# Optimization experiments

Hardware: AMD Instinct MI355X
Metric: run time of the kernel (lower is better)

The kernel has to match this reference:

```python
import jax, jax.numpy as jnp
import numpy as np
from jax.ops import segment_sum

N_NODES = 100000
N_EDGES = 1600000

def setup_inputs() -> dict:
    key = jax.random.key(0)
    ks = jax.random.split(key, 16)
    s = 0.1
    return {
        "x": jax.random.normal(ks[0], (N_NODES, 8), jnp.float32),
        "edge_index": jax.random.randint(ks[1], (2, N_EDGES), 0, N_NODES, jnp.int32),
        "W1l": jax.random.normal(ks[2], (8, 128)) * s,
        "W1r": jax.random.normal(ks[3], (8, 128)) * s,
        "b1": jnp.zeros((128,)),
        "W2l": jax.random.normal(ks[4], (128, 128)) * s,
        "W2r": jax.random.normal(ks[5], (128, 128)) * s,
        "b2": jnp.zeros((128,)),
        "W3l": jax.random.normal(ks[6], (128, 1)) * s,
        "W3r": jax.random.normal(ks[7], (128, 1)) * s,
        "b3": jnp.zeros((1,)),
        "Ta1_W": jax.random.normal(ks[8], (4, 8, 8)) * s,
        "Ta1_b": jnp.zeros((8,)),
        "Ta2_W": jax.random.normal(ks[9], (4, 8, 1)) * s,
        "Ta2_b": jnp.zeros((1,)),
        "Tb1_W": jax.random.normal(ks[10], (10, 8, 8)) * s,
        "Tb1_b": jnp.zeros((8,)),
        "Tb2_W": jax.random.normal(ks[11], (10, 8, 1)) * s,
        "Tb2_b": jnp.zeros((1,)),
        "lin2_W": jax.random.normal(ks[12], (2, 1)) * s,
        "lin2_b": jnp.zeros((1,)),
        "lin1_W": jax.random.normal(ks[13], (2, 1)) * s,
        "lin1_b": jnp.zeros((1,)),
    }

def reference(x, edge_index, W1l, W1r, b1, W2l, W2r, b2, W3l, W3r, b3,
              Ta1_W, Ta1_b, Ta2_W, Ta2_b, Tb1_W, Tb1_b, Tb2_W, Tb2_b,
              lin2_W, lin2_b, lin1_W, lin1_b):
    N = x.shape[0]
    src, dst = edge_index[0], edge_index[1]  # message flows src -> dst

    # in-degree of each target node (edge weight = 1)
    deg = segment_sum(jnp.ones_like(src, dtype=x.dtype), dst, num_segments=N)

    # --- SAGEConv: lin_l(mean_{j in N(i)} x_j) + lin_r(x_i) + bias ---
    inv_deg = jnp.where(deg > 0, 1.0 / jnp.maximum(deg, 1.0), 0.0)
    def sage(h, Wl, Wr, b):
        agg = segment_sum(h[src], dst, num_segments=N) * inv_deg[:, None]
        return agg @ Wl + h @ Wr + b

    # --- TAGConv: sym-normalized adjacency powers, no self loops ---
    dinv = jnp.where(deg > 0, jax.lax.rsqrt(jnp.maximum(deg, 1.0)), 0.0)
    norm = dinv[src] * dinv[dst]  # [E]
    def tag(h, Ws, b):  # Ws: [K+1, in, out]
        out = h @ Ws[0]
        for k in range(1, Ws.shape[0]):
            h = segment_sum(h[src] * norm[:, None], dst, num_segments=N)
            out = out + h @ Ws[k]
        return out + b

    relu = jax.nn.relu
    x1 = relu(sage(x, W1l, W1r, b1))
    x1 = relu(sage(x1, W2l, W2r, b2))
    x1 = relu(sage(x1, W3l, W3r, b3))

    x2 = relu(tag(x, Ta1_W, Ta1_b))
    x2 = relu(tag(x2, Ta2_W, Ta2_b))

    x3 = relu(tag(x, Tb1_W, Tb1_b))
    x3 = relu(tag(x3, Tb2_W, Tb2_b))

    x23 = relu(jnp.concatenate([x2, x3], axis=1) @ lin2_W + lin2_b)
    out = relu(jnp.concatenate([x1, x23], axis=1) @ lin1_W + lin1_b)
    return out
```

## Files before the change

### kernel.cpp

```cpp
#include <hip/hip_runtime.h>

#define NN 100000
#define NE 1600000
#define TPB 256

__global__ void k_init(int* __restrict__ deg, int* __restrict__ cursor, int* __restrict__ counter) {
    int i = blockIdx.x * TPB + threadIdx.x;
    if (i < NN) { deg[i] = 0; cursor[i] = 0; }
    if (i == 0) counter[0] = 0;
}

__global__ void k_deg(const int* __restrict__ dst, int* __restrict__ deg) {
    int e = blockIdx.x * TPB + threadIdx.x;
    if (e < NE) atomicAdd(&deg[dst[e]], 1);
}

__global__ void k_prep(const int* __restrict__ deg, float* __restrict__ inv_deg,
                       float* __restrict__ dinv, int* __restrict__ row_start,
                       int* __restrict__ counter) {
    int i = blockIdx.x * TPB + threadIdx.x;
    if (i < NN) {
        int d = deg[i];
        inv_deg[i] = d > 0 ? 1.0f / (float)d : 0.0f;
        dinv[i]    = d > 0 ? 1.0f / sqrtf((float)d) : 0.0f;
        row_start[i] = atomicAdd(counter, d);
    }
}

__global__ void k_fill(const int* __restrict__ src, const int* __restrict__ dst,
                       const int* __restrict__ row_start, int* __restrict__ cursor,
                       int* __restrict__ col) {
    int e = blockIdx.x * TPB + threadIdx.x;
    if (e < NE) {
        int d = dst[e];
        int p = atomicAdd(&cursor[d], 1);
        col[row_start[d] + p] = src[e];
    }
}

__global__ void k_meanprop8(const float* __restrict__ h, const int* __restrict__ row_start,
                            const int* __restrict__ deg, const float* __restrict__ inv_deg,
                            const int* __restrict__ col, float* __restrict__ out) {
    int t = blockIdx.x * TPB + threadIdx.x;
    if (t >= NN * 2) return;
    int n = t >> 1, half = t & 1;
    int rs = row_start[n], end = rs + deg[n];
    const float4* h4 = (const float4*)h;
    float4 s0 = make_float4(0,0,0,0), s1 = make_float4(0,0,0,0);
    int e = rs + half;
    for (; e + 2 < end; e += 4) {
        int c0 = col[e] * 2, c1 = col[e + 2] * 2;
        float4 a0 = h4[c0], a1 = h4[c0 + 1], b0 = h4[c1], b1 = h4[c1 + 1];
        s0.x += a0.x + b0.x; s0.y += a0.y + b0.y; s0.z += a0.z + b0.z; s0.w += a0.w + b0.w;
        s1.x += a1.x + b1.x; s1.y += a1.y + b1.y; s1.z += a1.z + b1.z; s1.w += a1.w + b1.w;
    }
    if (e < end) {
        int c0 = col[e] * 2;
        float4 a0 = h4[c0], a1 = h4[c0 + 1];
        s0.x += a0.x; s0.y += a0.y; s0.z += a0.z; s0.w += a0.w;
        s1.x += a1.x; s1.y += a1.y; s1.z += a1.z; s1.w += a1.w;
    }
    s0.x += __shfl_xor(s0.x, 1, 64); s0.y += __shfl_xor(s0.y, 1, 64);
    s0.z += __shfl_xor(s0.z, 1, 64); s0.w += __shfl_xor(s0.w, 1, 64);
    s1.x += __shfl_xor(s1.x, 1, 64); s1.y += __shfl_xor(s1.y, 1, 64);
    s1.z += __shfl_xor(s1.z, 1, 64); s1.w += __shfl_xor(s1.w, 1, 64);
    float w = inv_deg[n];
    float4 o = (half == 0) ? s0 : s1;
    o.x *= w; o.y *= w; o.z *= w; o.w *= w;
    ((float4*)out)[n * 2 + half] = o;
}

__global__ void k_meanprop128(const float* __restrict__ h, const int* __restrict__ row_start,
                              const int* __restrict__ deg, const float* __restrict__ inv_deg,
                              const int* __restrict__ col, float* __restrict__ out) {
    int t = blockIdx.x * TPB + threadIdx.x;
    if (t >= NN * 32) return;
    int n = t >> 5, f4 = t & 31;
    int rs = row_start[n], end = rs + deg[n];
    const float4* h4 = (const float4*)h;
    float4 s = make_float4(0.f, 0.f, 0.f, 0.f);
    int e = rs;
    for (; e + 1 < end; e += 2) {
        float4 v0 = h4[(size_t)col[e] * 32 + f4];
        float4 v1 = h4[(size_t)col[e + 1] * 32 + f4];
        s.x += v0.x + v1.x; s.y += v0.y + v1.y;
        s.z += v0.z + v1.z; s.w += v0.w + v1.w;
    }
    if (e < end) {
        float4 v = h4[(size_t)col[e] * 32 + f4];
        s.x += v.x; s.y += v.y; s.z += v.z; s.w += v.w;
    }
    float w = inv_deg[n];
    s.x *= w; s.y *= w; s.z *= w; s.w *= w;
    ((float4*)out)[t] = s;
}

__global__ void k_tagstep(const float* __restrict__ q, const int* __restrict__ row_start,
                          const int* __restrict__ deg, const float* __restrict__ dinv,
                          const int* __restrict__ col, float* __restrict__ qout,
                          const float* __restrict__ Wa, const float* __restrict__ Wb,
                          float* __restrict__ outa, float* __restrict__ outb,
                          const float* __restrict__ ba, const float* __restrict__ bb,
                          int fina, int finb) {
    int t = blockIdx.x * TPB + threadIdx.x;
    if (t >= NN * 4) return;
    int n = t >> 2, qd = t & 3;
    int rs = row_start[n], end = rs + deg[n];
    const float4* q4 = (const float4*)q;
    float4 s0 = make_float4(0,0,0,0), s1 = make_float4(0,0,0,0);
    int e = rs + qd;
    for (; e + 4 < end; e += 8) {
        int c0 = col[e] * 2, c1 = col[e + 4] * 2;
        float4 a0 = q4[c0], a1 = q4[c0 + 1], b0 = q4[c1], b1 = q4[c1 + 1];
        s0.x += a0.x + b0.x; s0.y += a0.y + b0.y; s0.z += a0.z + b0.z; s0.w += a0.w + b0.w;
        s1.x += a1.x + b1.x; s1.y += a1.y + b1.y; s1.z += a1.z + b1.z; s1.w += a1.w + b1.w;
    }
    if (e < end) {
        int c0 = col[e] * 2;
        float4 a0 = q4[c0], a1 = q4[c0 + 1];
        s0.x += a0.x; s0.y += a0.y; s0.z += a0.z; s0.w += a0.w;
        s1.x += a1.x; s1.y += a1.y; s1.z += a1.z; s1.w += a1.w;
    }
    #pragma unroll
    for (int o = 1; o < 4; o <<= 1) {
        s0.x += __shfl_xor(s0.x, o, 64); s0.y += __shfl_xor(s0.y, o, 64);
        s0.z += __shfl_xor(s0.z, o, 64); s0.w += __shfl_xor(s0.w, o, 64);
        s1.x += __shfl_xor(s1.x, o, 64); s1.y += __shfl_xor(s1.y, o, 64);
        s1.z += __shfl_xor(s1.z, o, 64); s1.w += __shfl_xor(s1.w, o, 64);
    }
    float dn = dinv[n];
    float h[8] = { s0.x * dn, s0.y * dn, s0.z * dn, s0.w * dn,
                   s1.x * dn, s1.y * dn, s1.z * dn, s1.w * dn };
    int f0 = qd * 2;
    if (qout) {
        ((float2*)qout)[n * 4 + qd] = make_float2(h[f0] * dn, h[f0 + 1] * dn);
    }
    if (Wa) {
        float2 o = ((float2*)outa)[n * 4 + qd];
        float v0 = o.x, v1 = o.y;
        #pragma unroll
        for (int j = 0; j < 8; ++j) {
            v0 += h[j] * Wa[j * 8 + f0];
            v1 += h[j] * Wa[j * 8 + f0 + 1];
        }
        if (fina) {
            v0 = fmaxf(v0 + ba[f0], 0.f);
            v1 = fmaxf(v1 + ba[f0 + 1], 0.f);
        }
        ((float2*)outa)[n * 4 + qd] = make_float2(v0, v1);
    }
    {
        float2 o = ((float2*)outb)[n * 4 + qd];
        float v0 = o.x, v1 = o.y;
        #pragma unroll
        for (int j = 0; j < 8; ++j) {
            v0 += h[j] * Wb[j * 8 + f0];
            v1 += h[j] * Wb[j * 8 + f0 + 1];
        }
        if (finb) {
            v0 = fmaxf(v0 + bb[f0], 0.f);
            v1 = fmaxf(v1 + bb[f0 + 1], 0.f);
        }
        ((float2*)outb)[n * 4 + qd] = make_float2(v0, v1);
    }
}

__global__ void k_symprop1n(const float* __restrict__ qin, const float* __restrict__ yk,
                            const int* __restrict__ row_start, const int* __restrict__ deg,
                            const float* __restrict__ dinv, const int* __restrict__ col,
                            float* __restrict__ qout, int qstride) {
    int t = blockIdx.x * TPB + threadIdx.x;
    if (t >= NN * 4) return;
    int n = t >> 2, qd = t & 3;
    int rs = row_start[n], d = deg[n];
    float s = 0.f;
    for (int e = rs + qd; e < rs + d; e += 4) s += qin[col[e]];
    s += __shfl_xor(s, 1, 64);
    s += __shfl_xor(s, 2, 64);
    if (qd == 0) {
        float dn = dinv[n];
        qout[(size_t)n * qstride] = dn * (dn * s + yk[n]);
    }
}

__global__ void k_symprop2(const float* __restrict__ q2in, const float* __restrict__ yka,
                           const float* __restrict__ ykb, const int* __restrict__ row_start,
                           const int* __restrict__ deg, const float* __restrict__ dinv,
                           const int* __restrict__ col, float* __restrict__ q2out) {
    int t = blockIdx.x * TPB + threadIdx.x;
    if (t >= NN * 4) return;
    int n = t >> 2, qd = t & 3;
    int rs = row_start[n], d = deg[n];
    const float2* q2 = (const float2*)q2in;
    float sa = 0.f, sb = 0.f;
    for (int e = rs + qd; e < rs + d; e += 4) {
        float2 v = q2[col[e]];
        sa += v.x; sb += v.y;
    }
    sa += __shfl_xor(sa, 1, 64); sa += __shfl_xor(sa, 2, 64);
    sb += __shfl_xor(sb, 1, 64); sb += __shfl_xor(sb, 2, 64);
    if (qd == 0) {
        float dn = dinv[n];
        ((float2*)q2out)[n] = make_float2(dn * (dn * sa + yka[n]),
                                          dn * (dn * sb + ykb[n]));
    }
}

__global__ void k_symprop2fin(const float* __restrict__ q2in, const float* __restrict__ yka,
                              const float* __restrict__ ykb, const int* __restrict__ row_start,
                              const int* __restrict__ deg, const float* __restrict__ dinv,
                              const int* __restrict__ col,
                              const float* __restrict__ biasa, const float* __restrict__ biasb,
                              const float* __restrict__ x1f,
                              const float* __restrict__ l2w, const float* __restrict__ l2b,
                              const float* __restrict__ l1w, const float* __restrict__ l1b,
                              float* __restrict__ out) {
    int t = blockIdx.x * TPB + threadIdx.x;
    if (t >= NN * 4) return;
    int n = t >> 2, qd = t & 3;
    int rs = row_start[n], d = deg[n];
    const float2* q2 = (const float2*)q2in;
    float sa = 0.f, sb = 0.f;
    for (int e = rs + qd; e < rs + d; e += 4) {
        float2 v = q2[col[e]];
        sa += v.x; sb += v.y;
    }
    sa += __shfl_xor(sa, 1, 64); sa += __shfl_xor(sa, 2, 64);
    sb += __shfl_xor(sb, 1, 64); sb += __shfl_xor(sb, 2, 64);
    if (qd == 0) {
        float dn = dinv[n];
        float x2 = fmaxf(dn * sa + yka[n] + biasa[0], 0.f);
        float x3 = fmaxf(dn * sb + ykb[n] + biasb[0], 0.f);
        float x23 = fmaxf(x2 * l2w[0] + x3 * l2w[1] + l2b[0], 0.f);
        out[n] = fmaxf(x1f[n] * l1w[0] + x23 * l1w[1] + l1b[0], 0.f);
    }
}

__global__ void k_red4(const float* __restrict__ ylp, const float* __restrict__ yrp,
                       float* __restrict__ yl, float* __restrict__ yr) {
    int n = blockIdx.x * TPB + threadIdx.x;
    if (n >= NN) return;
    yl[n] = (ylp[n] + ylp[NN + n]) + (ylp[2 * NN + n] + ylp[3 * NN + n]);
    yr[n] = (yrp[n] + yrp[NN + n]) + (yrp[2 * NN + n] + yrp[3 * NN + n]);
}

__global__ void k_sage3(const float* __restrict__ yl, const float* __restrict__ yr,
                        const int* __restrict__ row_start, const int* __restrict__ deg,
                        const float* __restrict__ inv_deg, const int* __restrict__ col,
                        const float* __restrict__ b3, float* __restrict__ x1f) {
    int t = blockIdx.x * TPB + threadIdx.x;
    if (t >= NN * 4) return;
    int n = t >> 2, q = t & 3;
    int rs = row_start[n], d = deg[n];
    float s = 0.f;
    for (int e = rs + q; e < rs + d; e += 4) s += yl[col[e]];
    s += __shfl_xor(s, 1, 64);
    s += __shfl_xor(s, 2, 64);
    if (q == 0) x1f[n] = fmaxf(s * inv_deg[n] + yr[n] + b3[0], 0.f);
}

__global__ void k_sage1(const float* __restrict__ a8, const float* __restrict__ x,
                        const float* __restrict__ W1l, const float* __restrict__ W1r,
                        const float* __restrict__ b1, float* __restrict__ x1) {
    int t = blockIdx.x * TPB + threadIdx.x;
    if (t >= NN * 16) return;
    int n = t >> 4, og = (t & 15) * 8;
    float acc[8];
    #pragma unroll
    for (int j = 0; j < 8; ++j) acc[j] = b1[og + j];
    const float* ar = a8 + (size_t)n * 8;
    const float* xr = x + (size_t)n * 8;
    #pragma unroll
    for (int k = 0; k < 8; ++k) {
        float av = ar[k], xv = xr[k];
        const float4* wl = (const float4*)(W1l + k * 128 + og);
        const float4* wr = (const float4*)(W1r + k * 128 + og);
        float4 l0 = wl[0], l1 = wl[1], r0 = wr[0], r1 = wr[1];
        acc[0] += av * l0.x + xv * r0.x;
        acc[1] += av * l0.y + xv * r0.y;
        acc[2] += av * l0.z + xv * r0.z;
        acc[3] += av * l0.w + xv * r0.w;
        acc[4] += av * l1.x + xv * r1.x;
        acc[5] += av * l1.y + xv * r1.y;
        acc[6] += av * l1.z + xv * r1.z;
        acc[7] += av * l1.w + xv * r1.w;
    }
    #pragma unroll
    for (int j = 0; j < 8; ++j)
        x1[(size_t)n * 128 + og + j] = fmaxf(acc[j], 0.f);
}

__global__ __launch_bounds__(256) void k_transpose(const float* __restrict__ in0,
        float* __restrict__ out0, const float* __restrict__ in1, float* __restrict__ out1) {
    const float* in = blockIdx.y ? in1 : in0;
    float* outp = blockIdx.y ? out1 : out0;
    __shared__ float t[128][65];
    int n0 = blockIdx.x * 64;
    int tid = threadIdx.x;
    #pragma unroll
    for (int i = 0; i < 8; ++i) {
        int idx = tid + i * 256;
        int nl = idx >> 5;
        int kq = (idx & 31) << 2;
        int n = n0 + nl;
        float4 v = (n < NN) ? *(const float4*)(in + (size_t)n * 128 + kq)
                            : make_float4(0.f, 0.f, 0.f, 0.f);
        t[kq][nl] = v.x; t[kq + 1][nl] = v.y; t[kq + 2][nl] = v.z; t[kq + 3][nl] = v.w;
    }
    __syncthreads();
    #pragma unroll
    for (int i = 0; i < 8; ++i) {
        int idx = tid + i * 256;
        int k = idx >> 4;
        int nq = (idx & 15) << 2;
        if (n0 + nq + 3 < NN) {
            float4 v = make_float4(t[k][nq], t[k][nq + 1], t[k][nq + 2], t[k][nq + 3]);
            *(float4*)(outp + (size_t)k * NN + n0 + nq) = v;
        }
    }
}

__global__ __launch_bounds__(256) void k_sage2f(const float* __restrict__ aT,
        const float* __restrict__ xT, const float* __restrict__ W2l,
        const float* __restrict__ W2r, const float* __restrict__ b2,
        const float* __restrict__ W3l, const float* __restrict__ W3r,
        float* __restrict__ ylp, float* __restrict__ yrp) {
    int xcd = blockIdx.x & 7;
    int s = blockIdx.x >> 3;
    int xblk = xcd * 49 + (s >> 2);
    int ogq = s & 3;
    int og = ogq * 32;
    int n0 = xblk * 256 + threadIdx.x;
    int n = (n0 < NN) ? n0 : (NN - 1);
    float acc[32];
    #pragma unroll
    for (int j = 0; j < 32; ++j) acc[j] = b2[og + j];
    const float* ap = aT + n;
    const float* xp = xT + n;
    const float* wlp = W2l + og;
    const float* wrp = W2r + og;
    #pragma unroll 4
    for (int k = 0; k < 128; ++k) {
        float a = ap[0], xv = xp[0];
        ap += NN; xp += NN;
        const float4* wl4 = (const float4*)(wlp + (k << 7));
        const float4* wr4 = (const float4*)(wrp + (k << 7));
        #pragma unroll
        for (int q = 0; q < 8; ++q) {
            float4 wl = wl4[q], wr = wr4[q];
            acc[q * 4 + 0] += a * wl.x + xv * wr.x;
            acc[q * 4 + 1] += a * wl.y + xv * wr.y;
            acc[q * 4 + 2] += a * wl.z + xv * wr.z;
            acc[q * 4 + 3] += a * wl.w + xv * wr.w;
        }
    }
    float pl = 0.f, pr = 0.f;
    #pragma unroll
    for (int j = 0; j < 32; ++j) {
        float v = fmaxf(acc[j], 0.f);
        pl += v * W3l[og + j];
        pr += v * W3r[og + j];
    }
    if (n0 < NN) {
        ylp[(size_t)ogq * NN + n0] = pl;
        yrp[(size_t)ogq * NN + n0] = pr;
    }
}

__global__ void k_taginit(const float* __restrict__ x, const float* __restrict__ TaW,
                          const float* __restrict__ TbW, const float* __restrict__ dinv,
                          float* __restrict__ outa, float* __restrict__ outb,
                          float* __restrict__ q0) {
    int t = blockIdx.x * TPB + threadIdx.x;
    if (t >= NN * 8) return;
    int n = t >> 3, o = t & 7;
    const float* xr = x + (size_t)n * 8;
    float sa = 0.f, sb = 0.f;
    #pragma unroll
    for (int j = 0; j < 8; ++j) {
        float v = xr[j];
        sa += v * TaW[j * 8 + o];
        sb += v * TbW[j * 8 + o];
    }
    outa[t] = sa;
    outb[t] = sb;
    q0[t] = xr[o] * dinv[n];
}

__global__ void k_tag2projAB(const float* __restrict__ outa, const float* __restrict__ outb,
                             const float* __restrict__ TaW2, const float* __restrict__ TbW2,
                             float* __restrict__ ya, float* __restrict__ yb,
                             const float* __restrict__ dinv,
                             float* __restrict__ q2a, float* __restrict__ qb0) {
    int n = blockIdx.x * TPB + threadIdx.x;
    if (n >= NN) return;
    float dn = dinv[n];
    float ha[8], hb[8];
    #pragma unroll
    for (int j = 0; j < 8; ++j) ha[j] = outa[(size_t)n * 8 + j];
    #pragma unroll
    for (int j = 0; j < 8; ++j) hb[j] = outb[(size_t)n * 8 + j];
    #pragma unroll
    for (int k = 0; k < 4; ++k) {
        float s = 0.f;
        #pragma unroll
        for (int j = 0; j < 8; ++j) s += ha[j] * TaW2[k * 8 + j];
        if (k == 3) q2a[(size_t)n * 2] = s * dn;
        else        ya[(size_t)k * NN + n] = s;
    }
    #pragma unroll
    for (int k = 0; k < 10; ++k) {
        float s = 0.f;
        #pragma unroll
        for (int j = 0; j < 8; ++j) s += hb[j] * TbW2[k * 8 + j];
        if (k == 9) qb0[n] = s * dn;
        else        yb[(size_t)k * NN + n] = s;
    }
}

#define GL(kern, n, ...) \
    kern<<<dim3((unsigned)(((long)(n) + TPB - 1) / TPB)), dim3(TPB), 0, stream>>>(__VA_ARGS__)

extern "C" void kernel_launch(void* const* d_in, const int* in_sizes, int n_in,
                              void* d_out, int out_size, void* d_ws, size_t ws_size,
                              hipStream_t stream) {
    (void)in_sizes; (void)n_in; (void)out_size; (void)ws_size;
    const float* x   = (const float*)d_in[0];
    const int*   ei  = (const int*)d_in[1];
    const int*   src = ei;
    const int*   dst = ei + NE;
    const float* W1l = (const float*)d_in[2];
    const float* W1r = (const float*)d_in[3];
    const float* b1  = (const float*)d_in[4];
    const float* W2l = (const float*)d_in[5];
    const float* W2r = (const float*)d_in[6];
    const float* b2  = (const float*)d_in[7];
    const float* W3l = (const float*)d_in[8];
    const float* W3r = (const float*)d_in[9];
    const float* b3  = (const float*)d_in[10];
    const float* TaW1 = (const float*)d_in[11];
    const float* TaB1 = (const float*)d_in[12];
    const float* TaW2 = (const float*)d_in[13];
    const float* TaB2 = (const float*)d_in[14];
    const float* TbW1 = (const float*)d_in[15];
    const float* TbB1 = (const float*)d_in[16];
    const float* TbW2 = (const float*)d_in[17];
    const float* TbB2 = (const float*)d_in[18];
    const float* l2w = (const float*)d_in[19];
    const float* l2b = (const float*)d_in[20];
    const float* l1w = (const float*)d_in[21];
    const float* l1b = (const float*)d_in[22];
    float* out = (float*)d_out;

    char* p = (char*)d_ws;
    size_t off = 0;
    auto alloc = [&](size_t bytes) -> void* {
        void* r = p + off;
        off = (off + bytes + 255) & ~(size_t)255;
        return r;
    };
    int*   deg       = (int*)  alloc((size_t)NN * 4);
    float* inv_deg   = (float*)alloc((size_t)NN * 4);
    float* dinv      = (float*)alloc((size_t)NN * 4);
    int*   row_start = (int*)  alloc((size_t)NN * 4);
    int*   cursor    = (int*)  alloc((size_t)NN * 4);
    int*   counter   = (int*)  alloc(256);
    int*   col       = (int*)  alloc((size_t)NE * 4);
    float* a8        = (float*)alloc((size_t)NN * 8 * 4);
    float* qA        = (float*)alloc((size_t)NN * 8 * 4);
    float* qB        = (float*)alloc((size_t)NN * 8 * 4);
    float* outa      = (float*)alloc((size_t)NN * 8 * 4);
    float* outb      = (float*)alloc((size_t)NN * 8 * 4);
    float* x1        = (float*)alloc((size_t)NN * 128 * 4);
    float* a128      = (float*)alloc((size_t)NN * 128 * 4);
    float* a128T     = (float*)alloc((size_t)NN * 128 * 4);
    float* x1T       = (float*)alloc((size_t)NN * 128 * 4);
    float* ylp       = (float*)alloc((size_t)NN * 4 * 4);
    float* yrp       = (float*)alloc((size_t)NN * 4 * 4);
    float* yl        = (float*)alloc((size_t)NN * 4);
    float* yr        = (float*)alloc((size_t)NN * 4);
    float* x1f       = (float*)alloc((size_t)NN * 4);
    float* tA        = (float*)alloc((size_t)NN * 4);
    float* tB        = (float*)alloc((size_t)NN * 4);
    float* qb0       = (float*)alloc((size_t)NN * 4);
    float* q2a       = (float*)alloc((size_t)NN * 8);
    float* q2b       = (float*)alloc((size_t)NN * 8);
    float* ya        = (float*)alloc((size_t)NN * 4 * 4);
    float* yb        = (float*)alloc((size_t)NN * 10 * 4);

    GL(k_init, NN, deg, cursor, counter);
    GL(k_deg, NE, dst, deg);
    GL(k_prep, NN, deg, inv_deg, dinv, row_start, counter);
    GL(k_fill, NE, src, dst, row_start, cursor, col);

    GL(k_meanprop8, (long)NN * 2, x, row_start, deg, inv_deg, col, a8);
    GL(k_sage1, (long)NN * 16, a8, x, W1l, W1r, b1, x1);
    GL(k_meanprop128, (long)NN * 32, x1, row_start, deg, inv_deg, col, a128);
    k_transpose<<<dim3((NN + 63) / 64, 2), dim3(256), 0, stream>>>(a128, a128T, x1, x1T);
    k_sage2f<<<dim3(1568), dim3(256), 0, stream>>>(a128T, x1T, W2l, W2r, b2, W3l, W3r, ylp, yrp);
    GL(k_red4, NN, ylp, yrp, yl, yr);
    GL(k_sage3, (long)NN * 4, yl, yr, row_start, deg, inv_deg, col, b3, x1f);

    GL(k_taginit, (long)NN * 8, x, TaW1, TbW1, dinv, outa, outb, qA);
    {
        float* qcur = qA;
        float* qnext = qB;
        for (int k = 1; k <= 9; ++k) {
            float* qout = (k < 9) ? qnext : nullptr;
            const float* Wa = (k <= 3) ? (TaW1 + (size_t)k * 64) : nullptr;
            GL(k_tagstep, (long)NN * 4, qcur, row_start, deg, dinv, col, qout,
               Wa, TbW1 + (size_t)k * 64, outa, outb, TaB1, TbB1,
               (k == 3) ? 1 : 0, (k == 9) ? 1 : 0);
            if (qout) { float* tmp = qcur; qcur = qnext; qnext = tmp; }
        }
    }

    GL(k_tag2projAB, NN, outa, outb, TaW2, TbW2, ya, yb, dinv, q2a, qb0);

    GL(k_symprop1n, (long)NN * 4, qb0, yb + 8 * NN, row_start, deg, dinv, col, tA, 1);
    GL(k_symprop1n, (long)NN * 4, tA,  yb + 7 * NN, row_start, deg, dinv, col, tB, 1);
    GL(k_symprop1n, (long)NN * 4, tB,  yb + 6 * NN, row_start, deg, dinv, col, tA, 1);
    GL(k_symprop1n, (long)NN * 4, tA,  yb + 5 * NN, row_start, deg, dinv, col, tB, 1);
    GL(k_symprop1n, (long)NN * 4, tB,  yb + 4 * NN, row_start, deg, dinv, col, tA, 1);
    GL(k_symprop1n, (long)NN * 4, tA,  yb + 3 * NN, row_start, deg, dinv, col, q2a + 1, 2);

    GL(k_symprop2, (long)NN * 4, q2a, ya + 2 * NN, yb + 2 * NN, row_start, deg, dinv, col, q2b);
    GL(k_symprop2, (long)NN * 4, q2b, ya + 1 * NN, yb + 1 * NN, row_start, deg, dinv, col, q2a);
    GL(k_symprop2fin, (long)NN * 4, q2a, ya + 0 * NN, yb + 0 * NN, row_start, deg, dinv, col,
       TaB2, TbB2, x1f, l2w, l2b, l1w, l1b, out);
}
```

Measured before the change: 779.8 us.

## Widen per-node thread groups to 8 lanes and split dense SAGE output groups

The edge-gather kernels (tagstep, symprop, sage3) now assign 8 threads per node instead of 4, which gives more parallelism and memory-level concurrency on the irregular gathers. In tagstep each lane now loads one float4 half rather than both halves. The SAGE2 fused matmul is split into 8 output groups of 16 instead of 4 of 32, doubling the block count and reducing register pressure, at the cost of a larger partial reduction. Row-start assignment in prep now uses a wavefront scan with one atomic per wave instead of one atomic per node.

```diff
diff --git a/kernel.cpp b/kernel.cpp
--- a/kernel.cpp
+++ b/kernel.cpp
@@ -19,11 +19,22 @@
                        float* __restrict__ dinv, int* __restrict__ row_start,
                        int* __restrict__ counter) {
     int i = blockIdx.x * TPB + threadIdx.x;
+    int lane = threadIdx.x & 63;
+    int d = (i < NN) ? deg[i] : 0;
+    int incl = d;
+    #pragma unroll
+    for (int o = 1; o < 64; o <<= 1) {
+        int v = __shfl_up(incl, o, 64);
+        if (lane >= o) incl += v;
+    }
+    int total = __shfl(incl, 63, 64);
+    int base = 0;
+    if (lane == 63) base = atomicAdd(counter, total);
+    base = __shfl(base, 63, 64);
     if (i < NN) {
-        int d = deg[i];
+        row_start[i] = base + incl - d;
         inv_deg[i] = d > 0 ? 1.0f / (float)d : 0.0f;
         dinv[i]    = d > 0 ? 1.0f / sqrtf((float)d) : 0.0f;
-        row_start[i] = atomicAdd(counter, d);
     }
 }
 
@@ -103,65 +114,56 @@
                           const float* __restrict__ ba, const float* __restrict__ bb,
                           int fina, int finb) {
     int t = blockIdx.x * TPB + threadIdx.x;
-    if (t >= NN * 4) return;
-    int n = t >> 2, qd = t & 3;
+    if (t >= NN * 8) return;
+    int n = t >> 3, qd = t & 7;
+    int half = qd & 1, epar = qd >> 1;
     int rs = row_start[n], end = rs + deg[n];
     const float4* q4 = (const float4*)q;
-    float4 s0 = make_float4(0,0,0,0), s1 = make_float4(0,0,0,0);
-    int e = rs + qd;
+    float4 s = make_float4(0,0,0,0);
+    int e = rs + epar;
     for (; e + 4 < end; e += 8) {
-        int c0 = col[e] * 2, c1 = col[e + 4] * 2;
-        float4 a0 = q4[c0], a1 = q4[c0 + 1], b0 = q4[c1], b1 = q4[c1 + 1];
-        s0.x += a0.x + b0.x; s0.y += a0.y + b0.y; s0.z += a0.z + b0.z; s0.w += a0.w + b0.w;
-        s1.x += a1.x + b1.x; s1.y += a1.y + b1.y; s1.z += a1.z + b1.z; s1.w += a1.w + b1.w;
+        int c0 = col[e] * 2 + half, c1 = col[e + 4] * 2 + half;
+        float4 a = q4[c0], b = q4[c1];
+        s.x += a.x + b.x; s.y += a.y + b.y; s.z += a.z + b.z; s.w += a.w + b.w;
     }
     if (e < end) {
-        int c0 = col[e] * 2;
-        float4 a0 = q4[c0], a1 = q4[c0 + 1];
-        s0.x += a0.x; s0.y += a0.y; s0.z += a0.z; s0.w += a0.w;
-        s1.x += a1.x; s1.y += a1.y; s1.z += a1.z; s1.w += a1.w;
-    }
-    #pragma unroll
-    for (int o = 1; o < 4; o <<= 1) {
-        s0.x += __shfl_xor(s0.x, o, 64); s0.y += __shfl_xor(s0.y, o, 64);
-        s0.z += __shfl_xor(s0.z, o, 64); s0.w += __shfl_xor(s0.w, o, 64);
-        s1.x += __shfl_xor(s1.x, o, 64); s1.y += __shfl_xor(s1.y, o, 64);
-        s1.z += __shfl_xor(s1.z, o, 64); s1.w += __shfl_xor(s1.w, o, 64);
+        float4 a = q4[col[e] * 2 + half];
+        s.x += a.x; s.y += a.y; s.z += a.z; s.w += a.w;
+    }
+    #pragma unroll
+    for (int o = 2; o < 8; o <<= 1) {
+        s.x += __shfl_xor(s.x, o, 64); s.y += __shfl_xor(s.y, o, 64);
+        s.z += __shfl_xor(s.z, o, 64); s.w += __shfl_xor(s.w, o, 64);
     }
     float dn = dinv[n];
-    float h[8] = { s0.x * dn, s0.y * dn, s0.z * dn, s0.w * dn,
-                   s1.x * dn, s1.y * dn, s1.z * dn, s1.w * dn };
-    int f0 = qd * 2;
-    if (qout) {
-        ((float2*)qout)[n * 4 + qd] = make_float2(h[f0] * dn, h[f0 + 1] * dn);
-    }
+    float m0 = s.x * dn, m1 = s.y * dn, m2 = s.z * dn, m3 = s.w * dn;
+    if (qout && epar == 0) {
+        ((float4*)qout)[n * 2 + half] = make_float4(m0 * dn, m1 * dn, m2 * dn, m3 * dn);
+    }
+    float o0 = __shfl_xor(m0, 1, 64), o1 = __shfl_xor(m1, 1, 64);
+    float o2 = __shfl_xor(m2, 1, 64), o3 = __shfl_xor(m3, 1, 64);
+    float h[8];
+    if (half) {
+        h[0] = o0; h[1] = o1; h[2] = o2; h[3] = o3;
+        h[4] = m0; h[5] = m1; h[6] = m2; h[7] = m3;
+    } else {
+        h[0] = m0; h[1] = m1; h[2] = m2; h[3] = m3;
+        h[4] = o0; h[5] = o1; h[6] = o2; h[7] = o3;
+    }
+    int f = qd;
     if (Wa) {
-        float2 o = ((float2*)outa)[n * 4 + qd];
-        float v0 = o.x, v1 = o.y;
+        float v = outa[(size_t)n * 8 + f];
         #pragma unroll
-        for (int j = 0; j < 8; ++j) {
-            v0 += h[j] * Wa[j * 8 + f0];
-            v1 += h[j] * Wa[j * 8 + f0 + 1];
-        }
-        if (fina) {
-            v0 = fmaxf(v0 + ba[f0], 0.f);
-            v1 = fmaxf(v1 + ba[f0 + 1], 0.f);
-        }
-        ((float2*)outa)[n * 4 + qd] = make_float2(v0, v1);
+        for (int j = 0; j < 8; ++j) v += h[j] * Wa[j * 8 + f];
+        if (fina) v = fmaxf(v + ba[f], 0.f);
+        outa[(size_t)n * 8 + f] = v;
     }
     {
-        float2 o = ((float2*)outb)[n * 4 + qd];
-        float v0 = o.x, v1 = o.y;
+        float v = outb[(size_t)n * 8 + f];
         #pragma unroll
-        for (int j = 0; j < 8; ++j) {
-            v0 += h[j] * Wb[j * 8 + f0];
-            v1 += h[j] * Wb[j * 8 + f0 + 1];
-        }
-        if (finb) {
-            v0 = fmaxf(v0 + bb[f0], 0.f);
-            v1 = fmaxf(v1 + bb[f0 + 1], 0.f);
-        }
-        ((float2*)outb)[n * 4 + qd] = make_float2(v0, v1);
+        for (int j = 0; j < 8; ++j) v += h[j] * Wb[j * 8 + f];
+        if (finb) v = fmaxf(v + bb[f], 0.f);
+        outb[(size_t)n * 8 + f] = v;
     }
 }
 
@@ -170,13 +172,14 @@
                             const float* __restrict__ dinv, const int* __restrict__ col,
                             float* __restrict__ qout, int qstride) {
     int t = blockIdx.x * TPB + threadIdx.x;
-    if (t >= NN * 4) return;
-    int n = t >> 2, qd = t & 3;
+    if (t >= NN * 8) return;
+    int n = t >> 3, qd = t & 7;
     int rs = row_start[n], d = deg[n];
     float s = 0.f;
-    for (int e = rs + qd; e < rs + d; e += 4) s += qin[col[e]];
+    for (int e = rs + qd; e < rs + d; e += 8) s += qin[col[e]];
     s += __shfl_xor(s, 1, 64);
     s += __shfl_xor(s, 2, 64);
+    s += __shfl_xor(s, 4, 64);
     if (qd == 0) {
         float dn = dinv[n];
         qout[(size_t)n * qstride] = dn * (dn * s + yk[n]);
@@ -188,17 +191,17 @@
                            const int* __restrict__ deg, const float* __restrict__ dinv,
                            const int* __restrict__ col, float* __restrict__ q2out) {
     int t = blockIdx.x * TPB + threadIdx.x;
-    if (t >= NN * 4) return;
-    int n = t >> 2, qd = t & 3;
+    if (t >= NN * 8) return;
+    int n = t >> 3, qd = t & 7;
     int rs = row_start[n], d = deg[n];
     const float2* q2 = (const float2*)q2in;
     float sa = 0.f, sb = 0.f;
-    for (int e = rs + qd; e < rs + d; e += 4) {
+    for (int e = rs + qd; e < rs + d; e += 8) {
         float2 v = q2[col[e]];
         sa += v.x; sb += v.y;
     }
-    sa += __shfl_xor(sa, 1, 64); sa += __shfl_xor(sa, 2, 64);
-    sb += __shfl_xor(sb, 1, 64); sb += __shfl_xor(sb, 2, 64);
+    sa += __shfl_xor(sa, 1, 64); sa += __shfl_xor(sa, 2, 64); sa += __shfl_xor(sa, 4, 64);
+    sb += __shfl_xor(sb, 1, 64); sb += __shfl_xor(sb, 2, 64); sb += __shfl_xor(sb, 4, 64);
     if (qd == 0) {
         float dn = dinv[n];
         ((float2*)q2out)[n] = make_float2(dn * (dn * sa + yka[n]),
@@ -216,17 +219,17 @@
                               const float* __restrict__ l1w, const float* __restrict__ l1b,
                               float* __restrict__ out) {
     int t = blockIdx.x * TPB + threadIdx.x;
-    if (t >= NN * 4) return;
-    int n = t >> 2, qd = t & 3;
+    if (t >= NN * 8) return;
+    int n = t >> 3, qd = t & 7;
     int rs = row_start[n], d = deg[n];
     const float2* q2 = (const float2*)q2in;
     float sa = 0.f, sb = 0.f;
-    for (int e = rs + qd; e < rs + d; e += 4) {
+    for (int e = rs + qd; e < rs + d; e += 8) {
         float2 v = q2[col[e]];
         sa += v.x; sb += v.y;
     }
-    sa += __shfl_xor(sa, 1, 64); sa += __shfl_xor(sa, 2, 64);
-    sb += __shfl_xor(sb, 1, 64); sb += __shfl_xor(sb, 2, 64);
+    sa += __shfl_xor(sa, 1, 64); sa += __shfl_xor(sa, 2, 64); sa += __shfl_xor(sa, 4, 64);
+    sb += __shfl_xor(sb, 1, 64); sb += __shfl_xor(sb, 2, 64); sb += __shfl_xor(sb, 4, 64);
     if (qd == 0) {
         float dn = dinv[n];
         float x2 = fmaxf(dn * sa + yka[n] + biasa[0], 0.f);
@@ -236,12 +239,18 @@
     }
 }
 
-__global__ void k_red4(const float* __restrict__ ylp, const float* __restrict__ yrp,
+__global__ void k_red8(const float* __restrict__ ylp, const float* __restrict__ yrp,
                        float* __restrict__ yl, float* __restrict__ yr) {
     int n = blockIdx.x * TPB + threadIdx.x;
     if (n >= NN) return;
-    yl[n] = (ylp[n] + ylp[NN + n]) + (ylp[2 * NN + n] + ylp[3 * NN + n]);
-    yr[n] = (yrp[n] + yrp[NN + n]) + (yrp[2 * NN + n] + yrp[3 * NN + n]);
+    float sl = 0.f, sr = 0.f;
+    #pragma unroll
+    for (int j = 0; j < 8; ++j) {
+        sl += ylp[(size_t)j * NN + n];
+        sr += yrp[(size_t)j * NN + n];
+    }
+    yl[n] = sl;
+    yr[n] = sr;
 }
 
 __global__ void k_sage3(const float* __restrict__ yl, const float* __restrict__ yr,
@@ -249,13 +258,14 @@
                         const float* __restrict__ inv_deg, const int* __restrict__ col,
                         const float* __restrict__ b3, float* __restrict__ x1f) {
     int t = blockIdx.x * TPB + threadIdx.x;
-    if (t >= NN * 4) return;
-    int n = t >> 2, q = t & 3;
+    if (t >= NN * 8) return;
+    int n = t >> 3, q = t & 7;
     int rs = row_start[n], d = deg[n];
     float s = 0.f;
-    for (int e = rs + q; e < rs + d; e += 4) s += yl[col[e]];
+    for (int e = rs + q; e < rs + d; e += 8) s += yl[col[e]];
     s += __shfl_xor(s, 1, 64);
     s += __shfl_xor(s, 2, 64);
+    s += __shfl_xor(s, 4, 64);
     if (q == 0) x1f[n] = fmaxf(s * inv_deg[n] + yr[n] + b3[0], 0.f);
 }
 
@@ -327,14 +337,14 @@
         float* __restrict__ ylp, float* __restrict__ yrp) {
     int xcd = blockIdx.x & 7;
     int s = blockIdx.x >> 3;
-    int xblk = xcd * 49 + (s >> 2);
-    int ogq = s & 3;
-    int og = ogq * 32;
+    int xblk = xcd * 49 + (s >> 3);
+    int ogq = s & 7;
+    int og = ogq * 16;
     int n0 = xblk * 256 + threadIdx.x;
     int n = (n0 < NN) ? n0 : (NN - 1);
-    float acc[32];
-    #pragma unroll
-    for (int j = 0; j < 32; ++j) acc[j] = b2[og + j];
+    float acc[16];
+    #pragma unroll
+    for (int j = 0; j < 16; ++j) acc[j] = b2[og + j];
     const float* ap = aT + n;
     const float* xp = xT + n;
     const float* wlp = W2l + og;
@@ -346,7 +356,7 @@
         const float4* wl4 = (const float4*)(wlp + (k << 7));
         const float4* wr4 = (const float4*)(wrp + (k << 7));
         #pragma unroll
-        for (int q = 0; q < 8; ++q) {
+        for (int q = 0; q < 4; ++q) {
             float4 wl = wl4[q], wr = wr4[q];
             acc[q * 4 + 0] += a * wl.x + xv * wr.x;
             acc[q * 4 + 1] += a * wl.y + xv * wr.y;
@@ -356,7 +366,7 @@
     }
     float pl = 0.f, pr = 0.f;
     #pragma unroll
-    for (int j = 0; j < 32; ++j) {
+    for (int j = 0; j < 16; ++j) {
         float v = fmaxf(acc[j], 0.f);
         pl += v * W3l[og + j];
         pr += v * W3r[og + j];
@@ -475,8 +485,8 @@
     float* a128      = (float*)alloc((size_t)NN * 128 * 4);
     float* a128T     = (float*)alloc((size_t)NN * 128 * 4);
     float* x1T       = (float*)alloc((size_t)NN * 128 * 4);
-    float* ylp       = (float*)alloc((size_t)NN * 4 * 4);
-    float* yrp       = (float*)alloc((size_t)NN * 4 * 4);
+    float* ylp       = (float*)alloc((size_t)NN * 8 * 4);
+    float* yrp       = (float*)alloc((size_t)NN * 8 * 4);
     float* yl        = (float*)alloc((size_t)NN * 4);
     float* yr        = (float*)alloc((size_t)NN * 4);
     float* x1f       = (float*)alloc((size_t)NN * 4);
@@ -497,9 +507,9 @@
     GL(k_sage1, (long)NN * 16, a8, x, W1l, W1r, b1, x1);
     GL(k_meanprop128, (long)NN * 32, x1, row_start, deg, inv_deg, col, a128);
     k_transpose<<<dim3((NN + 63) / 64, 2), dim3(256), 0, stream>>>(a128, a128T, x1, x1T);
-    k_sage2f<<<dim3(1568), dim3(256), 0, stream>>>(a128T, x1T, W2l, W2r, b2, W3l, W3r, ylp, yrp);
-    GL(k_red4, NN, ylp, yrp, yl, yr);
-    GL(k_sage3, (long)NN * 4, yl, yr, row_start, deg, inv_deg, col, b3, x1f);
+    k_sage2f<<<dim3(3136), dim3(256), 0, stream>>>(a128T, x1T, W2l, W2r, b2, W3l, W3r, ylp, yrp);
+    GL(k_red8, NN, ylp, yrp, yl, yr);
+    GL(k_sage3, (long)NN * 8, yl, yr, row_start, deg, inv_deg, col, b3, x1f);
 
     GL(k_taginit, (long)NN * 8, x, TaW1, TbW1, dinv, outa, outb, qA);
     {
@@ -508,7 +518,7 @@
         for (int k = 1; k <= 9; ++k) {
             float* qout = (k < 9) ? qnext : nullptr;
             const float* Wa = (k <= 3) ? (TaW1 + (size_t)k * 64) : nullptr;
-            GL(k_tagstep, (long)NN * 4, qcur, row_start, deg, dinv, col, qout,
+            GL(k_tagstep, (long)NN * 8, qcur, row_start, deg, dinv, col, qout,
                Wa, TbW1 + (size_t)k * 64, outa, outb, TaB1, TbB1,
                (k == 3) ? 1 : 0, (k == 9) ? 1 : 0);
             if (qout) { float* tmp = qcur; qcur = qnext; qnext = tmp; }
@@ -517,15 +527,15 @@
 
     GL(k_tag2projAB, NN, outa, outb, TaW2, TbW2, ya, yb, dinv, q2a, qb0);
 
-    GL(k_symprop1n, (long)NN * 4, qb0, yb + 8 * NN, row_start, deg, dinv, col, tA, 1);
-    GL(k_symprop1n, (long)NN * 4, tA,  yb + 7 * NN, row_start, deg, dinv, col, tB, 1);
-    GL(k_symprop1n, (long)NN * 4, tB,  yb + 6 * NN, row_start, deg, dinv, col, tA, 1);
-    GL(k_symprop1n, (long)NN * 4, tA,  yb + 5 * NN, row_start, deg, dinv, col, tB, 1);
-    GL(k_symprop1n, (long)NN * 4, tB,  yb + 4 * NN, row_start, deg, dinv, col, tA, 1);
-    GL(k_symprop1n, (long)NN * 4, tA,  yb + 3 * NN, row_start, deg, dinv, col, q2a + 1, 2);
-
-    GL(k_symprop2, (long)NN * 4, q2a, ya + 2 * NN, yb + 2 * NN, row_start, deg, dinv, col, q2b);
-    GL(k_symprop2, (long)NN * 4, q2b, ya + 1 * NN, yb + 1 * NN, row_start, deg, dinv, col, q2a);
-    GL(k_symprop2fin, (long)NN * 4, q2a, ya + 0 * NN, yb + 0 * NN, row_start, deg, dinv, col,
+    GL(k_symprop1n, (long)NN * 8, qb0, yb + 8 * NN, row_start, deg, dinv, col, tA, 1);
+    GL(k_symprop1n, (long)NN * 8, tA,  yb + 7 * NN, row_start, deg, dinv, col, tB, 1);
+    GL(k_symprop1n, (long)NN * 8, tB,  yb + 6 * NN, row_start, deg, dinv, col, tA, 1);
+    GL(k_symprop1n, (long)NN * 8, tA,  yb + 5 * NN, row_start, deg, dinv, col, tB, 1);
+    GL(k_symprop1n, (long)NN * 8, tB,  yb + 4 * NN, row_start, deg, dinv, col, tA, 1);
+    GL(k_symprop1n, (long)NN * 8, tA,  yb + 3 * NN, row_start, deg, dinv, col, q2a + 1, 2);
+
+    GL(k_symprop2, (long)NN * 8, q2a, ya + 2 * NN, yb + 2 * NN, row_start, deg, dinv, col, q2b);
+    GL(k_symprop2, (long)NN * 8, q2b, ya + 1 * NN, yb + 1 * NN, row_start, deg, dinv, col, q2a);
+    GL(k_symprop2fin, (long)NN * 8, q2a, ya + 0 * NN, yb + 0 * NN, row_start, deg, dinv, col,
        TaB2, TbB2, x1f, l2w, l2b, l1w, l1b, out);
 }
```

Measured after the change: 765.9 us. No clear change (-1.8%).
